# Kernel optimization log

Measured on AMD Instinct MI355X. Metric: run time of the kernel, lower is better.

The kernel has to match this reference:

```python
import jax, jax.numpy as jnp
import numpy as np
import math

B, L, M, N, S = 1024, 32, 128, 4096, 32


def setup_inputs() -> dict:
    key = jax.random.key(0)
    k1, k2, k3 = jax.random.split(key, 3)
    k = jax.random.normal(k1, (B, L, M), dtype=jnp.float32)
    # kaiming-uniform-like init: U(-bound, bound)
    bound_e = math.sqrt(6.0 / (N * M))
    bound_d = math.sqrt(6.0 / (M * N))
    W_e = jax.random.uniform(k2, (L, N, M), dtype=jnp.float32, minval=-bound_e, maxval=bound_e)
    W_d = jax.random.uniform(k3, (L, M, N), dtype=jnp.float32, minval=-bound_d, maxval=bound_d)
    # decoder columns are unit-normalized along the m axis (dim=-2), as in __init__
    W_d = W_d / jnp.linalg.norm(W_d, axis=-2, keepdims=True)
    b_e = jnp.zeros((L, N), dtype=jnp.float32)
    b_d = jnp.zeros((L, M), dtype=jnp.float32)
    return {"k": k, "W_e": W_e, "b_e": b_e, "W_d": W_d, "b_d": b_d, "s": S}


def hard_thresholding(y, s):
    # keep the s largest-|.| activations per (batch, layer) row, zero the rest
    _, idx = jax.lax.top_k(jnp.abs(y), s)  # idx: [B, L, s]
    b, l, _ = y.shape
    mask = jnp.zeros_like(y).at[
        jnp.arange(b)[:, None, None], jnp.arange(l)[None, :, None], idx
    ].set(1.0)
    return y * mask


def reference(k, W_e, b_e, W_d, b_d, s):
    # NOTE: b_e is created by the module but (faithfully) unused in encode()
    k_bar = k - b_d                                  # [B, L, M]
    y = jnp.einsum('lnm,blm->bln', W_e, k_bar)        # [B, L, N]
    y = hard_thresholding(y, s)
    k_hat = jnp.einsum('lmn,bln->blm', W_d, y)        # [B, L, M]
    loss = jnp.mean((k_hat - k) ** 2)
    return (loss, k_hat, y)
```

## Files before the change

### kernel.cpp

```cpp
#include <hip/hip_runtime.h>
#include <hip/hip_bf16.h>

#define B_ 1024
#define L_ 32
#define M_ 128
#define N_ 4096
#define S_ 32
#define ROWS (B_ * L_)

typedef __attribute__((ext_vector_type(8))) short    short8_t;
typedef __attribute__((ext_vector_type(8))) unsigned short ushort8_t;
typedef __attribute__((ext_vector_type(4))) float    f32x4;
typedef __attribute__((ext_vector_type(4))) unsigned int uint4_t;

__device__ __forceinline__ unsigned short f2bf(float x) {
    unsigned u = __float_as_uint(x);
    unsigned r = (u + 0x7FFFu + ((u >> 16) & 1u)) >> 16;
    return (unsigned short)r;
}
__device__ __forceinline__ float bf2f(unsigned short h) {
    return __uint_as_float((unsigned)h << 16);
}

#define KEY_E0 14720

__global__ __launch_bounds__(256) void prologue(float* __restrict__ y,
                                                const float* __restrict__ We,
                                                const float* __restrict__ bd,
                                                unsigned short* __restrict__ Wbf,
                                                float* __restrict__ cvec,
                                                const float* __restrict__ kin,
                                                unsigned short* __restrict__ Abf,
                                                const float* __restrict__ Wd,
                                                float* __restrict__ WdT) {
    __shared__ float t[32][33];
    const int bid = blockIdx.x;
    const int tid = threadIdx.x;

    if (bid < 2048) {
        const int row0 = bid * 16;
        const float4 z = {0.f, 0.f, 0.f, 0.f};
        #pragma unroll
        for (int i = 0; i < 32; ++i) {
            int g = i * 256 + tid;
            int r = row0 + (g >> 9);
            int slot = g & 511;
            reinterpret_cast<float4*>(y + (size_t)r * N_)[slot] = z;
        }
        #pragma unroll
        for (int i = 0; i < 16; ++i) {
            int g = i * 256 + tid;
            int r = row0 + (g >> 8);
            int slot = g & 255;
            reinterpret_cast<float4*>(y + (size_t)r * N_ + 3072)[slot] = z;
        }
    } else if (bid < 10240) {
        int wb = bid - 2048;
        int l = wb >> 8, nb = wb & 255;
        int nl = tid >> 4, tt = tid & 15;
        int n = nb * 16 + nl;
        const float* w = We + ((size_t)l * N_ + n) * M_ + tt * 8;
        const float* b = bd + l * M_ + tt * 8;
        float4 w0 = *(const float4*)(w), w1 = *(const float4*)(w + 4);
        float4 b0 = *(const float4*)(b), b1 = *(const float4*)(b + 4);
        ushort8_t o;
        o[0] = f2bf(w0.x); o[1] = f2bf(w0.y); o[2] = f2bf(w0.z); o[3] = f2bf(w0.w);
        o[4] = f2bf(w1.x); o[5] = f2bf(w1.y); o[6] = f2bf(w1.z); o[7] = f2bf(w1.w);
        *reinterpret_cast<ushort8_t*>(Wbf + ((size_t)l * N_ + n) * 128 + tt * 8) = o;
        float s = w0.x*b0.x + w0.y*b0.y + w0.z*b0.z + w0.w*b0.w
                + w1.x*b1.x + w1.y*b1.y + w1.z*b1.z + w1.w*b1.w;
        #pragma unroll
        for (int oo = 8; oo > 0; oo >>= 1) s += __shfl_xor(s, oo, 64);
        if (tt == 0) cvec[(size_t)l * N_ + n] = s;
    } else if (bid < 26624) {
        int g = (bid - 10240) * 256 + tid;
        int b = g >> 12, l = (g >> 7) & 31, m = g & 127;
        Abf[(((size_t)l * B_ + b) << 7) + m] = f2bf(kin[g]);
    } else {
        int tb = bid - 26624;
        int l  = tb >> 9;
        int rem = tb & 511;
        int n0 = (rem & 127) * 32, m0 = (rem >> 7) * 32;
        int tx = tid & 31, ty = tid >> 5;
        const float* src = Wd + (size_t)l * M_ * N_;
        for (int i = ty; i < 32; i += 8)
            t[i][tx] = src[(size_t)(m0 + i) * N_ + n0 + tx];
        __syncthreads();
        float* dst = WdT + (size_t)l * N_ * M_;
        for (int i = ty; i < 32; i += 8)
            dst[(size_t)(n0 + i) * M_ + m0 + tx] = t[tx][i];
    }
}

__global__ __launch_bounds__(256) void transpose_wd(const float* __restrict__ Wd,
                                                    float* __restrict__ WdT) {
    __shared__ float t[32][33];
    int l = blockIdx.z;
    int n0 = blockIdx.x * 32, m0 = blockIdx.y * 32;
    int tx = threadIdx.x & 31, ty = threadIdx.x >> 5;
    const float* src = Wd + (size_t)l * M_ * N_;
    for (int i = ty; i < 32; i += 8)
        t[i][tx] = src[(size_t)(m0 + i) * N_ + n0 + tx];
    __syncthreads();
    float* dst = WdT + (size_t)l * N_ * M_;
    for (int i = ty; i < 32; i += 8)
        dst[(size_t)(n0 + i) * M_ + m0 + tx] = t[tx][i];
}

__device__ __forceinline__ int swz(int row) { return (row & 3) ^ ((row >> 2) & 3); }

#define CPB 144

__global__ __launch_bounds__(256) void encoder_mfma(const unsigned short* __restrict__ Abf,
                                                    const unsigned short* __restrict__ Wbf,
                                                    const float* __restrict__ cvec,
                                                    unsigned char* __restrict__ y8) {
    const int orig = ((blockIdx.x & 7) << 10) + (blockIdx.x >> 3);
    const int l    = orig >> 8;
    const int rem  = orig & 255;
    const int bn0  = (rem & 31) * 128;
    const int bm0  = (rem >> 5) * 128;
    __shared__ __align__(16) unsigned char smemB[128 * CPB];
    unsigned short* As = (unsigned short*)smemB;
    unsigned short* Bs = (unsigned short*)(smemB + 8192);
    const int tid  = threadIdx.x;
    const int lane = tid & 63, wave = tid >> 6;
    const int wr = wave >> 1, wc = wave & 1;

    const unsigned short* Ab = Abf + (((size_t)l * B_ + bm0) << 7);
    const unsigned short* Wb = Wbf + (((size_t)l * N_ + bn0) << 7);

    auto stage = [&](int k0) {
        #pragma unroll
        for (int i = 0; i < 2; ++i) {
            int p   = i * 256 + tid;
            int row = p >> 2;
            int lc  = (p & 3) ^ swz(row);
            const unsigned short* g = Ab + ((size_t)row << 7) + k0 + lc * 8;
            unsigned dst = (unsigned)((i * 256 + (tid & ~63)) * 16);
            __builtin_amdgcn_global_load_lds(
                (const __attribute__((address_space(1))) void*)g,
                (__attribute__((address_space(3))) void*)((char*)As + dst), 16, 0, 0);
        }
        #pragma unroll
        for (int i = 0; i < 2; ++i) {
            int p   = i * 256 + tid;
            int row = p >> 2;
            int lc  = (p & 3) ^ swz(row);
            const unsigned short* g = Wb + ((size_t)row << 7) + k0 + lc * 8;
            unsigned dst = (unsigned)((i * 256 + (tid & ~63)) * 16);
            __builtin_amdgcn_global_load_lds(
                (const __attribute__((address_space(1))) void*)g,
                (__attribute__((address_space(3))) void*)((char*)Bs + dst), 16, 0, 0);
        }
    };

    f32x4 acc[4][4];
    #pragma unroll
    for (int i = 0; i < 4; ++i)
        #pragma unroll
        for (int j = 0; j < 4; ++j) acc[i][j] = (f32x4){0.f, 0.f, 0.f, 0.f};

    stage(0);
    __syncthreads();

    #pragma unroll
    for (int t = 0; t < 4; ++t) {
        short8_t aF[4], bF[4];
        const int kg = lane >> 4;
        #pragma unroll
        for (int mt = 0; mt < 4; ++mt) {
            int row = wr * 64 + mt * 16 + (lane & 15);
            int pc  = kg ^ swz(row);
            aF[mt] = *reinterpret_cast<const short8_t*>(As + row * 32 + pc * 8);
        }
        #pragma unroll
        for (int nt = 0; nt < 4; ++nt) {
            int row = wc * 64 + nt * 16 + (lane & 15);
            int pc  = kg ^ swz(row);
            bF[nt] = *reinterpret_cast<const short8_t*>(Bs + row * 32 + pc * 8);
        }
        #pragma unroll
        for (int mt = 0; mt < 4; ++mt)
            #pragma unroll
            for (int nt = 0; nt < 4; ++nt)
                acc[mt][nt] = __builtin_amdgcn_mfma_f32_16x16x32_bf16(
                    aF[mt], bF[nt], acc[mt][nt], 0, 0, 0);

        if (t < 3) {
            __syncthreads();
            stage((t + 1) * 32);
            __syncthreads();
        }
    }

    __syncthreads();

    #pragma unroll
    for (int nt = 0; nt < 4; ++nt) {
        int nl = wc * 64 + nt * 16 + (lane & 15);
        float cj = cvec[(size_t)l * N_ + bn0 + nl];
        #pragma unroll
        for (int mt = 0; mt < 4; ++mt) {
            #pragma unroll
            for (int j = 0; j < 4; ++j) {
                int rl = wr * 64 + mt * 16 + (lane >> 4) * 4 + j;
                float v = acc[mt][nt][j] - cj;
                unsigned mag = (__float_as_uint(v) >> 16) & 0x7FFFu;
                int key = ((int)mag - KEY_E0) >> 3;
                key = key < 0 ? 0 : (key > 255 ? 255 : key);
                smemB[rl * CPB + nl] = (unsigned char)key;
            }
        }
    }
    __syncthreads();

    #pragma unroll
    for (int i = 0; i < 4; ++i) {
        int chunk = i * 256 + tid;
        int r = chunk >> 3, cch = chunk & 7;
        uint4_t v = *reinterpret_cast<const uint4_t*>(smemB + r * CPB + cch * 16);
        unsigned char* dst = y8 + ((size_t)((bm0 + r) * L_ + l)) * 16384 + 8192 + bn0 + cch * 16;
        *reinterpret_cast<uint4_t*>(dst) = v;
    }
}

#define POOL 128
#define MARGIN 1.2e-3f

__global__ __launch_bounds__(256) void topk_decode(float* __restrict__ y,
                                                   const float* __restrict__ We,
                                                   const float* __restrict__ WdT,
                                                   const float* __restrict__ kin,
                                                   const float* __restrict__ cvec,
                                                   int* __restrict__ cidx,
                                                   float* __restrict__ cval,
                                                   float* __restrict__ khat,
                                                   float* __restrict__ partial) {
    const int w    = threadIdx.x >> 6;
    const int lane = threadIdx.x & 63;
    const int i  = ((blockIdx.x & 7) << 10) + (blockIdx.x >> 3);
    const int p  = 3 - (i >> 11);
    const int x  = (i >> 8) & 7;
    const int l  = 4 * x + p;
    const int j  = i & 255;
    const int bm = 7 - (j >> 5);
    const int bq = j & 31;
    const int b  = bm * 128 + bq * 4 + w;
    const int row = b * L_ + l;

    __shared__ __align__(16) float kinS[4][M_];
    __shared__ int   pidxS[4][POOL];
    __shared__ float pexS[4][POOL];
    __shared__ int   sidxS[4][S_];
    __shared__ float svalS[4][S_];

    float* yo = y + (size_t)row * N_;
    const unsigned char* ya8 = (const unsigned char*)y + (size_t)row * 16384 + 8192;

    kinS[w][lane]      = kin[(size_t)row * M_ + lane];
    kinS[w][lane + 64] = kin[(size_t)row * M_ + lane + 64];

    unsigned ak[16];
    #pragma unroll
    for (int jj = 0; jj < 4; ++jj) {
        uint4_t q = *reinterpret_cast<const uint4_t*>(ya8 + jj * 1024 + lane * 16);
        #pragma unroll
        for (int d = 0; d < 4; ++d) ak[jj * 4 + d] = q[d];
    }

    unsigned mxk = 0u;
    #pragma unroll
    for (int ii = 0; ii < 16; ++ii) {
        unsigned v = ak[ii];
        mxk = max(mxk, v & 0xFFu);
        mxk = max(mxk, (v >> 8) & 0xFFu);
        mxk = max(mxk, (v >> 16) & 0xFFu);
        mxk = max(mxk, v >> 24);
    }
    #pragma unroll
    for (int o = 32; o > 0; o >>= 1)
        mxk = max(mxk, (unsigned)__shfl_xor((int)mxk, o, 64));

    unsigned lo = 0u, hi = mxk;
    int cl = N_;
    for (int it = 0; it < 12 && cl > 48 && lo < hi; ++it) {
        unsigned t = (it == 0) ? 121u : lo + ((hi - lo + 1u) >> 1);
        t = min(max(t, lo + 1u), hi);
        int c = 0;
        #pragma unroll
        for (int ii = 0; ii < 16; ++ii) {
            unsigned v = ak[ii];
            c += ((v & 0xFFu) >= t) ? 1 : 0;
            c += (((v >> 8) & 0xFFu) >= t) ? 1 : 0;
            c += (((v >> 16) & 0xFFu) >= t) ? 1 : 0;
            c += ((v >> 24) >= t) ? 1 : 0;
        }
        #pragma unroll
        for (int o = 32; o > 0; o >>= 1) c += __shfl_xor(c, o, 64);
        if (c >= S_) { lo = t; cl = c; } else { hi = t - 1u; }
    }

    const float lov = __uint_as_float((unsigned)(KEY_E0 + (int)(lo << 3)) << 16);
    const float thf = fmaxf(lov - MARGIN, 0.0f);
    int tht = ((int)((__float_as_uint(thf) >> 16) & 0x7FFFu) - KEY_E0) >> 3;
    const unsigned th = tht < 0 ? 0u : (unsigned)tht;

    int myc = 0;
    #pragma unroll
    for (int ii = 0; ii < 16; ++ii) {
        unsigned v = ak[ii];
        myc += ((v & 0xFFu) >= th) ? 1 : 0;
        myc += (((v >> 8) & 0xFFu) >= th) ? 1 : 0;
        myc += (((v >> 16) & 0xFFu) >= th) ? 1 : 0;
        myc += ((v >> 24) >= th) ? 1 : 0;
    }
    int pos = myc;
    #pragma unroll
    for (int o = 1; o < 64; o <<= 1) {
        int t = __shfl_up(pos, o, 64);
        if (lane >= o) pos += t;
    }
    const int base  = pos - myc;
    const int total = __shfl(pos, 63, 64);
    int k = 0;
    #pragma unroll
    for (int jj = 0; jj < 4; ++jj)
        #pragma unroll
        for (int d = 0; d < 4; ++d) {
            unsigned v = ak[jj * 4 + d];
            #pragma unroll
            for (int bb = 0; bb < 4; ++bb) {
                unsigned key = (v >> (bb * 8)) & 0xFFu;
                if (key >= th) {
                    int pp = base + k;
                    if (pp < POOL) pidxS[w][pp] = jj * 1024 + lane * 16 + d * 4 + bb;
                    ++k;
                }
            }
        }
    __asm__ __volatile__("s_waitcnt lgkmcnt(0)" ::: "memory");
    int c = total < POOL ? total : POOL;

    if (lane < c) {
        int n = pidxS[w][lane];
        const float4* wp4 = reinterpret_cast<const float4*>(We + ((size_t)l * N_ + n) * M_);
        const float4* kp4 = reinterpret_cast<const float4*>(kinS[w]);
        float acc = -cvec[(size_t)l * N_ + n];
        #pragma unroll 8
        for (int m4 = 0; m4 < 32; ++m4) {
            float4 wv = wp4[m4], kv = kp4[m4];
            acc = fmaf(wv.x, kv.x, acc);
            acc = fmaf(wv.y, kv.y, acc);
            acc = fmaf(wv.z, kv.z, acc);
            acc = fmaf(wv.w, kv.w, acc);
        }
        pexS[w][lane] = acc;
    }
    if (lane + 64 < c) {
        int n = pidxS[w][lane + 64];
        const float4* wp4 = reinterpret_cast<const float4*>(We + ((size_t)l * N_ + n) * M_);
        const float4* kp4 = reinterpret_cast<const float4*>(kinS[w]);
        float acc = -cvec[(size_t)l * N_ + n];
        #pragma unroll 8
        for (int m4 = 0; m4 < 32; ++m4) {
            float4 wv = wp4[m4], kv = kp4[m4];
            acc = fmaf(wv.x, kv.x, acc);
            acc = fmaf(wv.y, kv.y, acc);
            acc = fmaf(wv.z, kv.z, acc);
            acc = fmaf(wv.w, kv.w, acc);
        }
        pexS[w][lane + 64] = acc;
    }
    __asm__ __volatile__("s_waitcnt lgkmcnt(0)" ::: "memory");

    for (int e = lane; e < c; e += 64) {
        float ae = fabsf(pexS[w][e]);
        int   ne = pidxS[w][e];
        int rank = 0;
        for (int jj = 0; jj < c; ++jj) {
            float aj = fabsf(pexS[w][jj]);
            rank += ((aj > ae) || (aj == ae && pidxS[w][jj] < ne)) ? 1 : 0;
        }
        if (rank < S_) {
            sidxS[w][rank] = ne;
            svalS[w][rank] = pexS[w][e];
        }
    }
    __asm__ __volatile__("s_waitcnt lgkmcnt(0)" ::: "memory");

    if (lane < S_) {
        int n = sidxS[w][lane];
        float v = svalS[w][lane];
        cidx[(size_t)row * S_ + lane] = n;
        cval[(size_t)row * S_ + lane] = v;
        if (n < 2048 || n >= 3072) yo[n] = v;
    }

    const float* wt = WdT + (size_t)l * N_ * M_;
    float acc0 = 0.0f, acc1 = 0.0f;
    #pragma unroll 8
    for (int jj = 0; jj < S_; ++jj) {
        float v = svalS[w][jj];
        const float* wrp = wt + (size_t)sidxS[w][jj] * M_;
        acc0 = fmaf(v, wrp[lane], acc0);
        acc1 = fmaf(v, wrp[lane + 64], acc1);
    }
    khat[(size_t)row * M_ + lane]      = acc0;
    khat[(size_t)row * M_ + lane + 64] = acc1;
    float r0 = acc0 - kinS[w][lane];
    float r1 = acc1 - kinS[w][lane + 64];
    float s = r0 * r0 + r1 * r1;
    #pragma unroll
    for (int o = 32; o > 0; o >>= 1) s += __shfl_xor(s, o, 64);
    if (lane == 0) partial[row] = s;
}

__global__ __launch_bounds__(256) void finish_high(float* __restrict__ y,
                                                   const int* __restrict__ cidx,
                                                   const float* __restrict__ cval,
                                                   const float* __restrict__ partial,
                                                   float* __restrict__ out_loss) {
    const int bid = blockIdx.x;
    const int tid = threadIdx.x;
    if (bid == 2048) {
        __shared__ float red[256];
        float s = 0.0f;
        for (int i = tid; i < ROWS / 4; i += 256) {
            float4 v = reinterpret_cast<const float4*>(partial)[i];
            s += v.x + v.y + v.z + v.w;
        }
        red[tid] = s;
        __syncthreads();
        for (int off = 128; off > 0; off >>= 1) {
            if (tid < off) red[tid] += red[tid + off];
            __syncthreads();
        }
        if (tid == 0) out_loss[0] = red[0] / (float)((size_t)B_ * L_ * M_);
        return;
    }
    const int row0 = bid * 16;
    const float4 z = {0.f, 0.f, 0.f, 0.f};
    #pragma unroll
    for (int i = 0; i < 16; ++i) {
        int g = i * 256 + tid;
        int r = row0 + (g >> 8);
        int slot = g & 255;
        reinterpret_cast<float4*>(y + (size_t)r * N_ + 2048)[slot] = z;
    }
    __syncthreads();
    #pragma unroll
    for (int i = 0; i < 2; ++i) {
        int e = i * 256 + tid;
        int g = row0 * S_ + e;
        int n = cidx[g];
        if (n >= 2048 && n < 3072) {
            int r = row0 + (e >> 5);
            y[(size_t)r * N_ + n] = cval[g];
        }
    }
}

extern "C" void kernel_launch(void* const* d_in, const int* in_sizes, int n_in,
                              void* d_out, int out_size, void* d_ws, size_t ws_size,
                              hipStream_t stream) {
    const float* kin = (const float*)d_in[0];
    const float* We  = (const float*)d_in[1];
    const float* Wd  = (const float*)d_in[3];
    const float* bd  = (const float*)d_in[4];

    float* out   = (float*)d_out;
    float* loss  = out;
    float* khat  = out + 1;
    float* y_out = out + 1 + (size_t)B_ * L_ * M_;

    char* ws = (char*)d_ws;
    const bool wsBig = ws_size >= ((size_t)113u << 20);

    unsigned short* Wbf;
    unsigned short* Abf;
    int*   cidx;
    float* cval;
    float* cvec;
    float* partial;
    float* WdT;

    if (wsBig) {
        Wbf     = (unsigned short*)ws;
        Abf     = (unsigned short*)(ws + (32u << 20));
        cidx    = (int*)  (ws + (40u << 20));
        cval    = (float*)(ws + (44u << 20));
        cvec    = (float*)(ws + (48u << 20));
        partial = (float*)(ws + (48u << 20) + (512u << 10));
        WdT     = (float*)(ws + (49u << 20));
    } else {
        Wbf     = (unsigned short*)ws;
        Abf     = (unsigned short*)(ws + (64u << 20));
        cidx    = (int*)  (ws + (72u << 20));
        cval    = (float*)(ws + (76u << 20));
        cvec    = (float*)(ws + (80u << 20));
        partial = (float*)(ws + (81u << 20));
        WdT     = (float*)ws;
    }

    int nblocks = 26624 + (wsBig ? 16384 : 0);
    prologue<<<nblocks, 256, 0, stream>>>(y_out, We, bd, Wbf, cvec, kin, Abf, Wd, WdT);
    encoder_mfma<<<8192, 256, 0, stream>>>(Abf, Wbf, cvec, (unsigned char*)y_out);
    if (!wsBig)
        transpose_wd<<<dim3(N_ / 32, M_ / 32, L_), 256, 0, stream>>>(Wd, WdT);
    topk_decode<<<ROWS / 4, 256, 0, stream>>>(y_out, We, WdT, kin, cvec,
                                              cidx, cval, khat, partial);
    finish_high<<<2049, 256, 0, stream>>>(y_out, cidx, cval, partial, loss);
}
```

Measured before the change: 502.2 us.

## Store encoder keys in dedicated workspace when large enough, skip finish pass

When the workspace holds at least 241 MiB, the 8-bit encoder keys go to a separate 4096-byte-stride buffer instead of being packed into the third quarter of each y row. The prologue then zeroes all of y, topk_decode scatters every selected value directly, and the 2049-block finish_high pass is replaced by a single-block loss reduction. This removes the second zeroing and scatter pass over that y region but adds prologue stores and depends on the harness providing that much workspace.

```diff
diff --git a/kernel.cpp b/kernel.cpp
--- a/kernel.cpp
+++ b/kernel.cpp
@@ -32,7 +32,8 @@
                                                 const float* __restrict__ kin,
                                                 unsigned short* __restrict__ Abf,
                                                 const float* __restrict__ Wd,
-                                                float* __restrict__ WdT) {
+                                                float* __restrict__ WdT,
+                                                int fullZero) {
     __shared__ float t[32][33];
     const int bid = blockIdx.x;
     const int tid = threadIdx.x;
@@ -53,6 +54,15 @@
             int r = row0 + (g >> 8);
             int slot = g & 255;
             reinterpret_cast<float4*>(y + (size_t)r * N_ + 3072)[slot] = z;
+        }
+        if (fullZero) {
+            #pragma unroll
+            for (int i = 0; i < 16; ++i) {
+                int g = i * 256 + tid;
+                int r = row0 + (g >> 8);
+                int slot = g & 255;
+                reinterpret_cast<float4*>(y + (size_t)r * N_ + 2048)[slot] = z;
+            }
         }
     } else if (bid < 10240) {
         int wb = bid - 2048;
@@ -114,7 +124,8 @@
 __global__ __launch_bounds__(256) void encoder_mfma(const unsigned short* __restrict__ Abf,
                                                     const unsigned short* __restrict__ Wbf,
                                                     const float* __restrict__ cvec,
-                                                    unsigned char* __restrict__ y8) {
+                                                    unsigned char* __restrict__ kbase,
+                                                    int kstride, int koff) {
     const int orig = ((blockIdx.x & 7) << 10) + (blockIdx.x >> 3);
     const int l    = orig >> 8;
     const int rem  = orig & 255;
@@ -220,7 +231,7 @@
         int chunk = i * 256 + tid;
         int r = chunk >> 3, cch = chunk & 7;
         uint4_t v = *reinterpret_cast<const uint4_t*>(smemB + r * CPB + cch * 16);
-        unsigned char* dst = y8 + ((size_t)((bm0 + r) * L_ + l)) * 16384 + 8192 + bn0 + cch * 16;
+        unsigned char* dst = kbase + (size_t)((bm0 + r) * L_ + l) * kstride + koff + bn0 + cch * 16;
         *reinterpret_cast<uint4_t*>(dst) = v;
     }
 }
@@ -229,6 +240,9 @@
 #define MARGIN 1.2e-3f
 
 __global__ __launch_bounds__(256) void topk_decode(float* __restrict__ y,
+                                                   const unsigned char* __restrict__ kbase,
+                                                   int kstride, int koff,
+                                                   int loQ, int hiQ,
                                                    const float* __restrict__ We,
                                                    const float* __restrict__ WdT,
                                                    const float* __restrict__ kin,
@@ -256,7 +270,7 @@
     __shared__ float svalS[4][S_];
 
     float* yo = y + (size_t)row * N_;
-    const unsigned char* ya8 = (const unsigned char*)y + (size_t)row * 16384 + 8192;
+    const unsigned char* ya8 = kbase + (size_t)row * kstride + koff;
 
     kinS[w][lane]      = kin[(size_t)row * M_ + lane];
     kinS[w][lane + 64] = kin[(size_t)row * M_ + lane + 64];
@@ -394,7 +408,7 @@
         float v = svalS[w][lane];
         cidx[(size_t)row * S_ + lane] = n;
         cval[(size_t)row * S_ + lane] = v;
-        if (n < 2048 || n >= 3072) yo[n] = v;
+        if (n < loQ || n >= hiQ) yo[n] = v;
     }
 
     const float* wt = WdT + (size_t)l * N_ * M_;
@@ -461,6 +475,24 @@
     }
 }
 
+__global__ __launch_bounds__(256) void reduce_loss(const float* __restrict__ partial,
+                                                   float* __restrict__ out_loss) {
+    __shared__ float red[256];
+    int tid = threadIdx.x;
+    float s = 0.0f;
+    for (int i = tid; i < ROWS / 4; i += 256) {
+        float4 v = reinterpret_cast<const float4*>(partial)[i];
+        s += v.x + v.y + v.z + v.w;
+    }
+    red[tid] = s;
+    __syncthreads();
+    for (int off = 128; off > 0; off >>= 1) {
+        if (tid < off) red[tid] += red[tid + off];
+        __syncthreads();
+    }
+    if (tid == 0) out_loss[0] = red[0] / (float)((size_t)B_ * L_ * M_);
+}
+
 extern "C" void kernel_launch(void* const* d_in, const int* in_sizes, int n_in,
                               void* d_out, int out_size, void* d_ws, size_t ws_size,
                               hipStream_t stream) {
@@ -475,7 +507,8 @@
     float* y_out = out + 1 + (size_t)B_ * L_ * M_;
 
     char* ws = (char*)d_ws;
-    const bool wsBig = ws_size >= ((size_t)113u << 20);
+    const bool wsHuge = ws_size >= ((size_t)241u << 20);
+    const bool wsBig  = ws_size >= ((size_t)113u << 20);
 
     unsigned short* Wbf;
     unsigned short* Abf;
@@ -484,6 +517,8 @@
     float* cvec;
     float* partial;
     float* WdT;
+    unsigned char* keys;
+    int kstride, koff, loQ, hiQ;
 
     if (wsBig) {
         Wbf     = (unsigned short*)ws;
@@ -502,13 +537,28 @@
         partial = (float*)(ws + (81u << 20));
         WdT     = (float*)ws;
     }
+    if (wsHuge) {
+        keys = (unsigned char*)(ws + ((size_t)113u << 20));
+        kstride = 4096; koff = 0;
+        loQ = 0; hiQ = 0;
+    } else {
+        keys = (unsigned char*)y_out;
+        kstride = 16384; koff = 8192;
+        loQ = 2048; hiQ = 3072;
+    }
 
     int nblocks = 26624 + (wsBig ? 16384 : 0);
-    prologue<<<nblocks, 256, 0, stream>>>(y_out, We, bd, Wbf, cvec, kin, Abf, Wd, WdT);
-    encoder_mfma<<<8192, 256, 0, stream>>>(Abf, Wbf, cvec, (unsigned char*)y_out);
+    prologue<<<nblocks, 256, 0, stream>>>(y_out, We, bd, Wbf, cvec, kin, Abf,
+                                          Wd, WdT, wsHuge ? 1 : 0);
+    encoder_mfma<<<8192, 256, 0, stream>>>(Abf, Wbf, cvec, keys, kstride, koff);
     if (!wsBig)
         transpose_wd<<<dim3(N_ / 32, M_ / 32, L_), 256, 0, stream>>>(Wd, WdT);
-    topk_decode<<<ROWS / 4, 256, 0, stream>>>(y_out, We, WdT, kin, cvec,
+    topk_decode<<<ROWS / 4, 256, 0, stream>>>(y_out, keys, kstride, koff, loQ, hiQ,
+                                              We, WdT, kin, cvec,
                                               cidx, cval, khat, partial);
-    finish_high<<<2049, 256, 0, stream>>>(y_out, cidx, cval, partial, loss);
-}
+    if (wsHuge) {
+        reduce_loss<<<1, 256, 0, stream>>>(partial, loss);
+    } else {
+        finish_high<<<2049, 256, 0, stream>>>(y_out, cidx, cval, partial, loss);
+    }
+}
```

Result: faster. 485.1 us (-3.4%).
